# Kernel optimization log

Measured on AMD Instinct MI355X. Metric: run time of the kernel, lower is better.

Reference implementation:

```python
import jax, jax.numpy as jnp
import numpy as np

D_MODEL = 1024
N_HEADS = 16
D_HEAD = D_MODEL // N_HEADS
D_FF = 4096
EPS = 1e-6  # flax LayerNorm default


def setup_inputs() -> dict:
    key = jax.random.key(0)
    ks = jax.random.split(key, 16)
    s = 1.0 / np.sqrt(D_MODEL)
    inp = {
        'x':  jax.random.normal(ks[0], (4, 2048, D_MODEL), jnp.float32),
        'Wq': jax.random.normal(ks[1], (D_MODEL, D_MODEL), jnp.float32) * s,
        'bq': jnp.zeros((D_MODEL,), jnp.float32),
        'Wk': jax.random.normal(ks[2], (D_MODEL, D_MODEL), jnp.float32) * s,
        'bk': jnp.zeros((D_MODEL,), jnp.float32),
        'Wv': jax.random.normal(ks[3], (D_MODEL, D_MODEL), jnp.float32) * s,
        'bv': jnp.zeros((D_MODEL,), jnp.float32),
        'Wo': jax.random.normal(ks[4], (D_MODEL, D_MODEL), jnp.float32) * s,
        'W1': jax.random.normal(ks[5], (D_MODEL, D_FF), jnp.float32) * s,
        'b1': jnp.zeros((D_FF,), jnp.float32),
        'W2': jax.random.normal(ks[6], (D_FF, D_MODEL), jnp.float32) * (1.0 / np.sqrt(D_FF)),
        'b2': jnp.zeros((D_MODEL,), jnp.float32),
        'g1': jnp.ones((D_MODEL,), jnp.float32),
        'beta1': jnp.zeros((D_MODEL,), jnp.float32),
        'g2': jnp.ones((D_MODEL,), jnp.float32),
        'beta2': jnp.zeros((D_MODEL,), jnp.float32),
    }
    return inp


def _layernorm(x, g, b):
    mu = jnp.mean(x, axis=-1, keepdims=True)
    var = jnp.mean(jnp.square(x - mu), axis=-1, keepdims=True)
    return (x - mu) * jax.lax.rsqrt(var + EPS) * g + b


def _attention(x, Wq, bq, Wk, bk, Wv, bv, Wo):
    B, S, D = x.shape
    def split_heads(t):
        return t.reshape(B, S, N_HEADS, D_HEAD).transpose(0, 2, 1, 3)  # bhsd
    q = split_heads(x @ Wq + bq)
    k = split_heads(x @ Wk + bk)
    v = split_heads(x @ Wv + bv)
    scale = jnp.sqrt(jnp.float32(D_HEAD))
    scores = jnp.einsum('bhsd,bhtd->bhst', q, k) / scale
    causal = jnp.tril(jnp.ones((S, S), dtype=jnp.bool_))
    scores = jnp.where(causal, scores, jnp.finfo(scores.dtype).min)
    w = jax.nn.softmax(scores, axis=-1)
    out = jnp.einsum('bhst,bhtd->bhsd', w, v)
    out = out.transpose(0, 2, 1, 3).reshape(B, S, D)
    return out @ Wo  # o_proj has no bias


def reference(x, Wq, bq, Wk, bk, Wv, bv, Wo, W1, b1, W2, b2, g1, beta1, g2, beta2):
    normed = _layernorm(x, g1, beta1)
    x = x + _attention(normed, Wq, bq, Wk, bk, Wv, bv, Wo)
    normed = _layernorm(x, g2, beta2)
    h = jax.nn.gelu(normed @ W1 + b1)  # approximate tanh gelu, matching flax nn.gelu
    x = x + (h @ W2 + b2)
    return x
```

## Files before the change

### kernel.cpp

```cpp
#include <hip/hip_runtime.h>

#define SEQ 2048
#define NROWS 8192
#define NH 16
#define DHEAD 64
#define QLD 3072

typedef float f32x4 __attribute__((ext_vector_type(4)));
typedef __bf16 bf16x8 __attribute__((ext_vector_type(8)));

__device__ __forceinline__ unsigned short f2bf(float f) {
  union { float f; unsigned u; } v; v.f = f;
  unsigned r = v.u + 0x7fffu + ((v.u >> 16) & 1u);
  return (unsigned short)(r >> 16);
}

__device__ __forceinline__ void gl16(const void* g, void* l) {
  __builtin_amdgcn_global_load_lds((const __attribute__((address_space(1))) void*)g,
                                   (__attribute__((address_space(3))) void*)l, 16, 0, 0);
}

__device__ __forceinline__ float gelu_f(float x) {
  float t = 0.7978845608028654f * (x + 0.044715f * x * x * x);
  float e = __expf(2.0f * t);
  float th = 1.0f - 2.0f / (e + 1.0f);
  return 0.5f * x * (1.0f + th);
}

#define CVTPK(dst, lo, hi) asm("v_cvt_pk_bf16_f32 %0, %1, %2" : "=v"(dst) : "v"(lo), "v"(hi))

#if __has_builtin(__builtin_amdgcn_permlane32_swap)
#define P32SWAP(a, b, x, y) { auto _t = __builtin_amdgcn_permlane32_swap((a), (b), false, false); (x) = _t[0]; (y) = _t[1]; }
#else
#define P32SWAP(a, b, x, y) { unsigned _as = (unsigned)__shfl_xor((int)(a), 32, 64); \
  unsigned _bs = (unsigned)__shfl_xor((int)(b), 32, 64); \
  (x) = (l < 32) ? (a) : _bs; (y) = (l < 32) ? _as : (b); }
#endif
#if __has_builtin(__builtin_amdgcn_permlane16_swap)
#define P16SWAP(a, b, x, y) { auto _t = __builtin_amdgcn_permlane16_swap((a), (b), false, false); (x) = _t[0]; (y) = _t[1]; }
#else
#define P16SWAP(a, b, x, y) { unsigned _as = (unsigned)__shfl_xor((int)(a), 16, 64); \
  unsigned _bs = (unsigned)__shfl_xor((int)(b), 16, 64); \
  (x) = (l & 16) ? _bs : (a); (y) = (l & 16) ? (b) : _as; }
#endif

__global__ __launch_bounds__(256) void transpose_cvt(const float* __restrict__ W,
                                                     unsigned short* __restrict__ Wt,
                                                     int K, int N) {
  __shared__ float tile[32][33];
  const int tx = threadIdx.x, ty = threadIdx.y;
  const int n0 = blockIdx.x * 32, k0 = blockIdx.y * 32;
#pragma unroll
  for (int i = ty; i < 32; i += 8)
    tile[i][tx] = W[(size_t)(k0 + i) * N + n0 + tx];
  __syncthreads();
#pragma unroll
  for (int i = ty; i < 32; i += 8)
    Wt[(size_t)(n0 + i) * K + k0 + tx] = f2bf(tile[tx][i]);
}

__global__ __launch_bounds__(256) void concat_bias(const float* __restrict__ bq,
                                                   const float* __restrict__ bk,
                                                   const float* __restrict__ bv,
                                                   float* __restrict__ dst) {
  int i = blockIdx.x * 256 + threadIdx.x;
  if (i < 1024) dst[i] = bq[i];
  else if (i < 2048) dst[i] = bk[i - 1024];
  else if (i < 3072) dst[i] = bv[i - 2048];
}

__global__ __launch_bounds__(256) void layernorm_k(const float* __restrict__ x,
                                                   const float* __restrict__ g,
                                                   const float* __restrict__ b,
                                                   unsigned short* __restrict__ out) {
  const int row = blockIdx.x, tid = threadIdx.x;
  const float4 v = reinterpret_cast<const float4*>(x + (size_t)row * 1024)[tid];
  float s = v.x + v.y + v.z + v.w;
  float s2 = v.x * v.x + v.y * v.y + v.z * v.z + v.w * v.w;
#pragma unroll
  for (int d = 1; d < 64; d <<= 1) { s += __shfl_xor(s, d, 64); s2 += __shfl_xor(s2, d, 64); }
  __shared__ float ls[4], ls2[4];
  const int w = tid >> 6;
  if ((tid & 63) == 0) { ls[w] = s; ls2[w] = s2; }
  __syncthreads();
  s = ls[0] + ls[1] + ls[2] + ls[3];
  s2 = ls2[0] + ls2[1] + ls2[2] + ls2[3];
  const float mu = s * (1.0f / 1024.0f);
  const float var = s2 * (1.0f / 1024.0f) - mu * mu;
  const float rstd = rsqrtf(var + 1e-6f);
  const float4 gv = reinterpret_cast<const float4*>(g)[tid];
  const float4 bv = reinterpret_cast<const float4*>(b)[tid];
  ushort4 o;
  o.x = f2bf((v.x - mu) * rstd * gv.x + bv.x);
  o.y = f2bf((v.y - mu) * rstd * gv.y + bv.y);
  o.z = f2bf((v.z - mu) * rstd * gv.z + bv.z);
  o.w = f2bf((v.w - mu) * rstd * gv.w + bv.w);
  reinterpret_cast<ushort4*>(out + (size_t)row * 1024)[tid] = o;
}

enum { EP_BIAS = 1, EP_RES = 2, EP_GELU = 4, EP_BF16 = 8, EP_QSCALE = 16 };

template <int E>
__global__ __launch_bounds__(256, 2) void gemm_k(const unsigned short* __restrict__ A,
                                                 const unsigned short* __restrict__ Bt,
                                                 const float* __restrict__ bias,
                                                 const float* __restrict__ resid,
                                                 void* __restrict__ out,
                                                 int M, int N, int K) {
  __shared__ __align__(16) unsigned short As[2][128 * 32];
  __shared__ __align__(16) unsigned short Bs[2][128 * 32];
  const int tid = threadIdx.x;
  const int l = tid & 63, w = tid >> 6;
  const int wr = w >> 1, wc = w & 1;
  const int lr = l & 15, lg = l >> 4;
  const int bn = blockIdx.x, bm = blockIdx.y;
  const unsigned short* Ab = A + (size_t)(bm * 128) * K;
  const unsigned short* Bb = Bt + (size_t)(bn * 128) * K;
  const int srow = tid >> 2, scol = (tid & 3) * 8;

  f32x4 acc[4][4];
#pragma unroll
  for (int m = 0; m < 4; ++m)
#pragma unroll
    for (int n = 0; n < 4; ++n) acc[m][n] = 0.0f;

  const int nk = K >> 5;
  auto stage = [&](int buf, int t) {
    const unsigned short* a0 = Ab + (size_t)srow * K + t * 32 + scol;
    const unsigned short* b0 = Bb + (size_t)srow * K + t * 32 + scol;
    gl16(a0, &As[buf][tid * 8]);
    gl16(a0 + (size_t)64 * K, &As[buf][2048 + tid * 8]);
    gl16(b0, &Bs[buf][tid * 8]);
    gl16(b0 + (size_t)64 * K, &Bs[buf][2048 + tid * 8]);
  };
  stage(0, 0);
  for (int t = 0;;) {
    __syncthreads();
    if (t + 1 < nk) stage((t + 1) & 1, t + 1);
    const unsigned short* Ac = As[t & 1];
    const unsigned short* Bc = Bs[t & 1];
    bf16x8 af[4], bfr[4];
#pragma unroll
    for (int m = 0; m < 4; ++m)
      af[m] = *reinterpret_cast<const bf16x8*>(&Ac[(wr * 64 + m * 16 + lr) * 32 + lg * 8]);
#pragma unroll
    for (int n = 0; n < 4; ++n)
      bfr[n] = *reinterpret_cast<const bf16x8*>(&Bc[(wc * 64 + n * 16 + lr) * 32 + lg * 8]);
#pragma unroll
    for (int m = 0; m < 4; ++m)
#pragma unroll
      for (int n = 0; n < 4; ++n)
        acc[m][n] = __builtin_amdgcn_mfma_f32_16x16x32_bf16(af[m], bfr[n], acc[m][n], 0, 0, 0);
    if (++t == nk) break;
  }

  const int row0 = bm * 128 + wr * 64, col0 = bn * 128 + wc * 64;
#pragma unroll
  for (int m = 0; m < 4; ++m) {
#pragma unroll
    for (int n = 0; n < 4; ++n) {
      const int col = col0 + n * 16 + lr;
      float bc = 0.0f;
      if (E & EP_BIAS) bc = bias[col];
#pragma unroll
      for (int j = 0; j < 4; ++j) {
        const int row = row0 + m * 16 + lg * 4 + j;
        float v = acc[m][n][j] + bc;
        if (E & EP_RES) v += resid[(size_t)row * N + col];
        if (E & EP_GELU) v = gelu_f(v);
        if (E & EP_QSCALE) { if (col < 1024) v *= 0.125f; }
        if (E & EP_BF16) ((unsigned short*)out)[(size_t)row * N + col] = f2bf(v);
        else ((float*)out)[(size_t)row * N + col] = v;
      }
    }
  }
}

__global__ __launch_bounds__(512, 4) void attn_k(const unsigned short* __restrict__ qkv,
                                                 unsigned short* __restrict__ out) {
  __shared__ __align__(16) unsigned short Kl[2][4096];
  __shared__ __align__(16) unsigned short Vt[2][4096];
  const int tid = threadIdx.x;
  const int l = tid & 63, w = tid >> 6;
  const int lr = l & 15, lg = l >> 4;
  const int bh = blockIdx.y;
  const int b = bh >> 4, h = bh & 15;
  const size_t rowbase = (size_t)b * SEQ;
  char* klb = (char*)Kl;
  char* vtb = (char*)Vt;
  const int sg = tid & 15, dhg = tid >> 4;

  auto stageK = [&](int buf, int kb2) {
    const int r = (w << 3) + (l >> 3);
    const char* src = (const char*)(qkv + (rowbase + kb2 + r) * QLD + 1024 + h * 64)
                      + 16 * ((l & 7) ^ (l >> 3));
    gl16(src, klb + buf * 8192 + (w << 10) + (l << 4));
  };
  auto loadV = [&](int kb2, uint2* vr) {
    if (tid < 256) {
#pragma unroll
      for (int i = 0; i < 4; ++i)
        vr[i] = *reinterpret_cast<const uint2*>(
            qkv + (rowbase + kb2 + sg * 4 + i) * QLD + 2048 + h * 64 + dhg * 4);
    }
  };
  auto writeV = [&](int buf, const uint2* vr) {
    if (tid < 256) {
      char* vb = vtb + buf * 8192;
#pragma unroll
      for (int jj = 0; jj < 4; ++jj) {
        const int dh = dhg * 4 + jj;
        unsigned a0 = (jj < 2) ? vr[0].x : vr[0].y;
        unsigned a1 = (jj < 2) ? vr[1].x : vr[1].y;
        unsigned a2 = (jj < 2) ? vr[2].x : vr[2].y;
        unsigned a3 = (jj < 2) ? vr[3].x : vr[3].y;
        unsigned s01, s23;
        if (jj & 1) {
          s01 = (a0 >> 16) | (a1 & 0xffff0000u);
          s23 = (a2 >> 16) | (a3 & 0xffff0000u);
        } else {
          s01 = (a0 & 0xffffu) | (a1 << 16);
          s23 = (a2 & 0xffffu) | (a3 << 16);
        }
        const int bo = (dh * 128 + sg * 8) ^ ((dh & 7) << 4);
        uint2 p; p.x = s01; p.y = s23;
        *reinterpret_cast<uint2*>(vb + bo) = p;
      }
    }
  };

#pragma unroll 1
  for (int seg = 0; seg < 2; ++seg) {
    const int qt = seg ? (15 - blockIdx.x) : blockIdx.x;
    const int q0 = qt << 7;
    const int ktmax = 2 * qt + 1;
    const int qwmin = q0 + w * 16;
    const int qrow = qwmin + lr;

    bf16x8 qf[2];
#pragma unroll
    for (int ks = 0; ks < 2; ++ks)
      qf[ks] = *reinterpret_cast<const bf16x8*>(
          qkv + (rowbase + qrow) * QLD + h * 64 + ks * 32 + lg * 8);

    f32x4 oacc[4];
#pragma unroll
    for (int n = 0; n < 4; ++n) oacc[n] = 0.0f;
    float mrun = -1e30f, lrun = 0.0f;

    {
      stageK(0, 0);
      uint2 vr[4];
      loadV(0, vr);
      writeV(0, vr);
    }
    __syncthreads();

#pragma unroll 1
    for (int kt = 0; kt <= ktmax; ++kt) {
      const int cur = kt & 1, nb = cur ^ 1;
      const int kb = kt << 6;
      const bool more = kt < ktmax;
      const bool active = kb <= qwmin + 15;
      uint2 vr[4];
      if (more) { stageK(nb, (kt + 1) << 6); loadV((kt + 1) << 6, vr); }

      f32x4 sacc[4];
      if (active) {
#pragma unroll
        for (int ni = 0; ni < 4; ++ni) sacc[ni] = 0.0f;
        const char* kc = klb + cur * 8192;
        __builtin_amdgcn_s_setprio(1);
#pragma unroll
        for (int ks = 0; ks < 2; ++ks) {
#pragma unroll
          for (int ni = 0; ni < 4; ++ni) {
            const int r = ni * 16 + lr;
            const int bo = (r * 128 + ks * 64 + lg * 16) ^ ((lr & 7) << 4);
            bf16x8 kf = *reinterpret_cast<const bf16x8*>(kc + bo);
            sacc[ni] = __builtin_amdgcn_mfma_f32_16x16x32_bf16(kf, qf[ks], sacc[ni], 0, 0, 0);
          }
        }
        __builtin_amdgcn_s_setprio(0);

        if (kb + 63 > qwmin) {
#pragma unroll
          for (int ni = 0; ni < 4; ++ni)
#pragma unroll
            for (int j = 0; j < 4; ++j)
              if (kb + ni * 16 + lg * 4 + j > qrow) sacc[ni][j] = -1e30f;
        }

        float pm = sacc[0][0];
#pragma unroll
        for (int ni = 0; ni < 4; ++ni)
#pragma unroll
          for (int j = 0; j < 4; ++j) pm = fmaxf(pm, sacc[ni][j]);
        pm = fmaxf(pm, __shfl_xor(pm, 16, 64));
        pm = fmaxf(pm, __shfl_xor(pm, 32, 64));
        const float mnew = fmaxf(mrun, pm);
        const float alpha = __expf(mrun - mnew);
        mrun = mnew;
        float rs = 0.0f;
#pragma unroll
        for (int ni = 0; ni < 4; ++ni)
#pragma unroll
          for (int j = 0; j < 4; ++j) {
            const float p = __expf(sacc[ni][j] - mnew);
            sacc[ni][j] = p;
            rs += p;
          }
        rs += __shfl_xor(rs, 16, 64);
        rs += __shfl_xor(rs, 32, 64);
        lrun = lrun * alpha + rs;
#pragma unroll
        for (int n = 0; n < 4; ++n) oacc[n] *= alpha;
      }

      if (more) writeV(nb, vr);

      if (active) {
        const char* vc = vtb + cur * 8192;
#pragma unroll
        for (int ks2 = 0; ks2 < 2; ++ks2) {
          unsigned U0, U1, U2, U3, C0, C1, W0, W1, W2, W3;
          CVTPK(U0, sacc[2 * ks2][0], sacc[2 * ks2][1]);
          CVTPK(U1, sacc[2 * ks2][2], sacc[2 * ks2][3]);
          CVTPK(U2, sacc[2 * ks2 + 1][0], sacc[2 * ks2 + 1][1]);
          CVTPK(U3, sacc[2 * ks2 + 1][2], sacc[2 * ks2 + 1][3]);
          P32SWAP(U0, U2, C0, C1);
          P16SWAP(C0, C1, W0, W2);
          P32SWAP(U1, U3, C0, C1);
          P16SWAP(C0, C1, W1, W3);
          union { uint4 u; bf16x8 v; } pu;
          pu.u = make_uint4(W0, W1, W2, W3);
          __builtin_amdgcn_s_setprio(1);
#pragma unroll
          for (int n = 0; n < 4; ++n) {
            const int r = n * 16 + lr;
            const int bo = (r * 128 + ks2 * 64 + lg * 16) ^ ((lr & 7) << 4);
            bf16x8 vf = *reinterpret_cast<const bf16x8*>(vc + bo);
            oacc[n] = __builtin_amdgcn_mfma_f32_16x16x32_bf16(vf, pu.v, oacc[n], 0, 0, 0);
          }
          __builtin_amdgcn_s_setprio(0);
        }
      }
      __syncthreads();
    }

    const float inv = 1.0f / lrun;
#pragma unroll
    for (int n = 0; n < 4; ++n) {
      ushort4 o;
      o.x = f2bf(oacc[n][0] * inv);
      o.y = f2bf(oacc[n][1] * inv);
      o.z = f2bf(oacc[n][2] * inv);
      o.w = f2bf(oacc[n][3] * inv);
      *reinterpret_cast<ushort4*>(out + (rowbase + qrow) * 1024 + h * 64 + n * 16 + lg * 4) = o;
    }
  }
}

extern "C" void kernel_launch(void* const* d_in, const int* in_sizes, int n_in,
                              void* d_out, int out_size, void* d_ws, size_t ws_size,
                              hipStream_t stream) {
  const float* x   = (const float*)d_in[0];
  const float* Wq  = (const float*)d_in[1];
  const float* bq  = (const float*)d_in[2];
  const float* Wk  = (const float*)d_in[3];
  const float* bk  = (const float*)d_in[4];
  const float* Wv  = (const float*)d_in[5];
  const float* bv  = (const float*)d_in[6];
  const float* Wo  = (const float*)d_in[7];
  const float* W1  = (const float*)d_in[8];
  const float* b1  = (const float*)d_in[9];
  const float* W2  = (const float*)d_in[10];
  const float* b2  = (const float*)d_in[11];
  const float* g1  = (const float*)d_in[12];
  const float* be1 = (const float*)d_in[13];
  const float* g2  = (const float*)d_in[14];
  const float* be2 = (const float*)d_in[15];

  char* ws = (char*)d_ws;
  size_t off = 0;
  auto alloc = [&](size_t bytes) { char* p = ws + off; off += (bytes + 255) & ~(size_t)255; return p; };
  unsigned short* WqkvT = (unsigned short*)alloc((size_t)3072 * 1024 * 2);
  unsigned short* WoT   = (unsigned short*)alloc((size_t)1024 * 1024 * 2);
  unsigned short* W1T   = (unsigned short*)alloc((size_t)4096 * 1024 * 2);
  unsigned short* W2T   = (unsigned short*)alloc((size_t)1024 * 4096 * 2);
  float*          bqkv  = (float*)alloc((size_t)3072 * 4);
  unsigned short* normed = (unsigned short*)alloc((size_t)NROWS * 1024 * 2);
  unsigned short* qkvbuf = (unsigned short*)alloc((size_t)NROWS * 4096 * 2);
  unsigned short* attnb  = (unsigned short*)alloc((size_t)NROWS * 1024 * 2);
  float*          x1     = (float*)alloc((size_t)NROWS * 1024 * 4);

  const dim3 tb(32, 8);
  transpose_cvt<<<dim3(32, 32), tb, 0, stream>>>(Wq, WqkvT, 1024, 1024);
  transpose_cvt<<<dim3(32, 32), tb, 0, stream>>>(Wk, WqkvT + 1024 * 1024, 1024, 1024);
  transpose_cvt<<<dim3(32, 32), tb, 0, stream>>>(Wv, WqkvT + 2 * 1024 * 1024, 1024, 1024);
  transpose_cvt<<<dim3(32, 32), tb, 0, stream>>>(Wo, WoT, 1024, 1024);
  transpose_cvt<<<dim3(128, 32), tb, 0, stream>>>(W1, W1T, 1024, 4096);
  transpose_cvt<<<dim3(32, 128), tb, 0, stream>>>(W2, W2T, 4096, 1024);
  concat_bias<<<12, 256, 0, stream>>>(bq, bk, bv, bqkv);

  layernorm_k<<<NROWS, 256, 0, stream>>>(x, g1, be1, normed);
  gemm_k<(EP_BIAS | EP_BF16 | EP_QSCALE)><<<dim3(24, 64), 256, 0, stream>>>(normed, WqkvT, bqkv, nullptr, qkvbuf, NROWS, 3072, 1024);
  attn_k<<<dim3(8, 64), 512, 0, stream>>>(qkvbuf, attnb);
  gemm_k<EP_RES><<<dim3(8, 64), 256, 0, stream>>>(attnb, WoT, nullptr, x, x1, NROWS, 1024, 1024);
  layernorm_k<<<NROWS, 256, 0, stream>>>(x1, g2, be2, normed);
  gemm_k<(EP_BIAS | EP_GELU | EP_BF16)><<<dim3(32, 64), 256, 0, stream>>>(normed, W1T, b1, nullptr, qkvbuf, NROWS, 4096, 1024);
  gemm_k<(EP_BIAS | EP_RES)><<<dim3(8, 64), 256, 0, stream>>>(qkvbuf, W2T, b2, x1, d_out, NROWS, 1024, 4096);
}
```

Measured before the change: 553.2 us.

## Replace GEMM with 8-wave 256-row tiled kernel using swizzled LDS and phased pipeline

Replaces the 128x128, 4-wave bf16 GEMM with a 512-thread kernel that uses 256xBN tiles and K-steps of 64. LDS is XOR-swizzled to avoid bank conflicts, and the next tile's global-to-LDS loads are spread across three phases interleaved with MFMA quarters, with raised wave priority during MFMA. Block indices are remapped so that neighbouring workgroups share operands in cache. The aim is more data reuse per byte loaded and better overlap of loads with compute, at the cost of more registers, more LDS and more barriers per iteration.

```diff
diff --git a/kernel.cpp b/kernel.cpp
--- a/kernel.cpp
+++ b/kernel.cpp
@@ -43,6 +43,11 @@
   unsigned _bs = (unsigned)__shfl_xor((int)(b), 16, 64); \
   (x) = (l & 16) ? _bs : (a); (y) = (l & 16) ? (b) : _as; }
 #endif
+
+#define MEMFENCE asm volatile("" ::: "memory")
+#define BAR() do { MEMFENCE; __builtin_amdgcn_s_barrier(); MEMFENCE; } while (0)
+#define WAIT_LGKM0 asm volatile("s_waitcnt lgkmcnt(0)" ::: "memory")
+#define WAIT_VM0 asm volatile("s_waitcnt vmcnt(0)" ::: "memory")
 
 __global__ __launch_bounds__(256) void transpose_cvt(const float* __restrict__ W,
                                                      unsigned short* __restrict__ Wt,
@@ -100,63 +105,158 @@
 
 enum { EP_BIAS = 1, EP_RES = 2, EP_GELU = 4, EP_BF16 = 8, EP_QSCALE = 16 };
 
-template <int E>
-__global__ __launch_bounds__(256, 2) void gemm_k(const unsigned short* __restrict__ A,
-                                                 const unsigned short* __restrict__ Bt,
-                                                 const float* __restrict__ bias,
-                                                 const float* __restrict__ resid,
-                                                 void* __restrict__ out,
-                                                 int M, int N, int K) {
-  __shared__ __align__(16) unsigned short As[2][128 * 32];
-  __shared__ __align__(16) unsigned short Bs[2][128 * 32];
+template <int BN, int E>
+__global__ __launch_bounds__(512, 2) void gemm8_k(const unsigned short* __restrict__ A,
+                                                  const unsigned short* __restrict__ Bt,
+                                                  const float* __restrict__ bias,
+                                                  const float* __restrict__ resid,
+                                                  void* __restrict__ out,
+                                                  int M, int N, int K) {
+  constexpr int BM = 256;
+  constexpr int NWC = (BN == 256) ? 4 : 2;
+  constexpr int WM = (BN == 256) ? 128 : 64;
+  constexpr int MI = WM / 16;
+  constexpr int MQ = MI / 2;
+  __shared__ __align__(16) unsigned short As[2][BM * 64];
+  __shared__ __align__(16) unsigned short Bs[2][BN * 64];
+
   const int tid = threadIdx.x;
   const int l = tid & 63, w = tid >> 6;
-  const int wr = w >> 1, wc = w & 1;
   const int lr = l & 15, lg = l >> 4;
-  const int bn = blockIdx.x, bm = blockIdx.y;
-  const unsigned short* Ab = A + (size_t)(bm * 128) * K;
-  const unsigned short* Bb = Bt + (size_t)(bn * 128) * K;
-  const int srow = tid >> 2, scol = (tid & 3) * 8;
-
-  f32x4 acc[4][4];
-#pragma unroll
-  for (int m = 0; m < 4; ++m)
+  const int wr = w / NWC, wc = w % NWC;
+
+  const int gx = gridDim.x;
+  const int nwg = gx * gridDim.y;
+  int lin = blockIdx.y * gx + blockIdx.x;
+  lin = (lin & 7) * (nwg >> 3) + (lin >> 3);
+  const int bn = lin % gx, bm = lin / gx;
+
+  const unsigned short* Ab = A + (size_t)(bm * BM) * K;
+  const unsigned short* Bb = Bt + (size_t)(bn * BN) * K;
+
+  const int srow = l >> 3;
+  const int sslot = (l & 7) ^ (srow & 7);
+  auto stA = [&](int buf, int t, int seg) {
+    gl16((const char*)(Ab + (size_t)(seg * 8 + srow) * K + t * 64) + sslot * 16,
+         (char*)As[buf] + seg * 1024 + l * 16);
+  };
+  auto stB = [&](int buf, int t, int seg) {
+    gl16((const char*)(Bb + (size_t)(seg * 8 + srow) * K + t * 64) + sslot * 16,
+         (char*)Bs[buf] + seg * 1024 + l * 16);
+  };
+  auto stage = [&](int buf, int t, int p) {
+    if (BN == 256) {
+      if (p == 0)      { stA(buf, t, w); stA(buf, t, 8 + w);  stB(buf, t, w); }
+      else if (p == 1) { stA(buf, t, 16 + w); stA(buf, t, 24 + w); stB(buf, t, 8 + w); }
+      else if (p == 2) { stB(buf, t, 16 + w); stB(buf, t, 24 + w); }
+    } else {
+      if (p == 0)      { stA(buf, t, w); stB(buf, t, w); }
+      else if (p == 1) { stA(buf, t, 8 + w); stB(buf, t, 8 + w); }
+      else if (p == 2) { stA(buf, t, 16 + w); stA(buf, t, 24 + w); }
+    }
+  };
+  auto rdA = [&](int buf, int r, int ks) {
+    return *reinterpret_cast<const bf16x8*>(
+        (const char*)As[buf] + r * 128 + (((ks << 2) + lg) ^ (r & 7)) * 16);
+  };
+  auto rdB = [&](int buf, int r, int ks) {
+    return *reinterpret_cast<const bf16x8*>(
+        (const char*)Bs[buf] + r * 128 + (((ks << 2) + lg) ^ (r & 7)) * 16);
+  };
+
+  f32x4 acc[MI][4];
+#pragma unroll
+  for (int m = 0; m < MI; ++m)
 #pragma unroll
     for (int n = 0; n < 4; ++n) acc[m][n] = 0.0f;
 
-  const int nk = K >> 5;
-  auto stage = [&](int buf, int t) {
-    const unsigned short* a0 = Ab + (size_t)srow * K + t * 32 + scol;
-    const unsigned short* b0 = Bb + (size_t)srow * K + t * 32 + scol;
-    gl16(a0, &As[buf][tid * 8]);
-    gl16(a0 + (size_t)64 * K, &As[buf][2048 + tid * 8]);
-    gl16(b0, &Bs[buf][tid * 8]);
-    gl16(b0 + (size_t)64 * K, &Bs[buf][2048 + tid * 8]);
-  };
-  stage(0, 0);
-  for (int t = 0;;) {
-    __syncthreads();
-    if (t + 1 < nk) stage((t + 1) & 1, t + 1);
-    const unsigned short* Ac = As[t & 1];
-    const unsigned short* Bc = Bs[t & 1];
-    bf16x8 af[4], bfr[4];
-#pragma unroll
-    for (int m = 0; m < 4; ++m)
-      af[m] = *reinterpret_cast<const bf16x8*>(&Ac[(wr * 64 + m * 16 + lr) * 32 + lg * 8]);
-#pragma unroll
-    for (int n = 0; n < 4; ++n)
-      bfr[n] = *reinterpret_cast<const bf16x8*>(&Bc[(wc * 64 + n * 16 + lr) * 32 + lg * 8]);
-#pragma unroll
-    for (int m = 0; m < 4; ++m)
-#pragma unroll
-      for (int n = 0; n < 4; ++n)
-        acc[m][n] = __builtin_amdgcn_mfma_f32_16x16x32_bf16(af[m], bfr[n], acc[m][n], 0, 0, 0);
-    if (++t == nk) break;
+  const int NK = K >> 6;
+#pragma unroll
+  for (int p = 0; p < 3; ++p) stage(0, 0, p);
+  WAIT_VM0;
+  BAR();
+
+#pragma unroll 2
+  for (int kt = 0; kt < NK; ++kt) {
+    const int c = kt & 1, nb = c ^ 1;
+    const bool more = kt + 1 < NK;
+    bf16x8 a0[MQ][2], a1[MQ][2], b0[2][2], b1[2][2];
+
+#pragma unroll
+    for (int mi = 0; mi < MQ; ++mi)
+#pragma unroll
+      for (int ks = 0; ks < 2; ++ks) a0[mi][ks] = rdA(c, wr * WM + mi * 16 + lr, ks);
+#pragma unroll
+    for (int ni = 0; ni < 2; ++ni)
+#pragma unroll
+      for (int ks = 0; ks < 2; ++ks) b0[ni][ks] = rdB(c, wc * 64 + ni * 16 + lr, ks);
+    if (more) stage(nb, kt + 1, 0);
+    BAR();
+    WAIT_LGKM0;
+    __builtin_amdgcn_s_setprio(1);
+#pragma unroll
+    for (int mi = 0; mi < MQ; ++mi)
+#pragma unroll
+      for (int ni = 0; ni < 2; ++ni)
+#pragma unroll
+        for (int ks = 0; ks < 2; ++ks)
+          acc[mi][ni] = __builtin_amdgcn_mfma_f32_16x16x32_bf16(a0[mi][ks], b0[ni][ks], acc[mi][ni], 0, 0, 0);
+    __builtin_amdgcn_s_setprio(0);
+    BAR();
+
+#pragma unroll
+    for (int ni = 0; ni < 2; ++ni)
+#pragma unroll
+      for (int ks = 0; ks < 2; ++ks) b1[ni][ks] = rdB(c, wc * 64 + (2 + ni) * 16 + lr, ks);
+    if (more) stage(nb, kt + 1, 1);
+    BAR();
+    WAIT_LGKM0;
+    __builtin_amdgcn_s_setprio(1);
+#pragma unroll
+    for (int mi = 0; mi < MQ; ++mi)
+#pragma unroll
+      for (int ni = 0; ni < 2; ++ni)
+#pragma unroll
+        for (int ks = 0; ks < 2; ++ks)
+          acc[mi][2 + ni] = __builtin_amdgcn_mfma_f32_16x16x32_bf16(a0[mi][ks], b1[ni][ks], acc[mi][2 + ni], 0, 0, 0);
+    __builtin_amdgcn_s_setprio(0);
+    BAR();
+
+#pragma unroll
+    for (int mi = 0; mi < MQ; ++mi)
+#pragma unroll
+      for (int ks = 0; ks < 2; ++ks) a1[mi][ks] = rdA(c, wr * WM + (MQ + mi) * 16 + lr, ks);
+    if (more) stage(nb, kt + 1, 2);
+    BAR();
+    WAIT_LGKM0;
+    __builtin_amdgcn_s_setprio(1);
+#pragma unroll
+    for (int mi = 0; mi < MQ; ++mi)
+#pragma unroll
+      for (int ni = 0; ni < 2; ++ni)
+#pragma unroll
+        for (int ks = 0; ks < 2; ++ks)
+          acc[MQ + mi][ni] = __builtin_amdgcn_mfma_f32_16x16x32_bf16(a1[mi][ks], b0[ni][ks], acc[MQ + mi][ni], 0, 0, 0);
+    __builtin_amdgcn_s_setprio(0);
+    BAR();
+
+    __builtin_amdgcn_s_setprio(1);
+#pragma unroll
+    for (int mi = 0; mi < MQ; ++mi)
+#pragma unroll
+      for (int ni = 0; ni < 2; ++ni)
+#pragma unroll
+        for (int ks = 0; ks < 2; ++ks)
+          acc[MQ + mi][2 + ni] = __builtin_amdgcn_mfma_f32_16x16x32_bf16(a1[mi][ks], b1[ni][ks], acc[MQ + mi][2 + ni], 0, 0, 0);
+    __builtin_amdgcn_s_setprio(0);
+    WAIT_VM0;
+    BAR();
   }
 
-  const int row0 = bm * 128 + wr * 64, col0 = bn * 128 + wc * 64;
-#pragma unroll
-  for (int m = 0; m < 4; ++m) {
+  const int row0 = bm * BM + wr * WM;
+  const int col0 = bn * BN + wc * 64;
+#pragma unroll
+  for (int m = 0; m < MI; ++m) {
 #pragma unroll
     for (int n = 0; n < 4; ++n) {
       const int col = col0 + n * 16 + lr;
@@ -404,10 +504,10 @@
   concat_bias<<<12, 256, 0, stream>>>(bq, bk, bv, bqkv);
 
   layernorm_k<<<NROWS, 256, 0, stream>>>(x, g1, be1, normed);
-  gemm_k<(EP_BIAS | EP_BF16 | EP_QSCALE)><<<dim3(24, 64), 256, 0, stream>>>(normed, WqkvT, bqkv, nullptr, qkvbuf, NROWS, 3072, 1024);
+  gemm8_k<256, (EP_BIAS | EP_BF16 | EP_QSCALE)><<<dim3(12, 32), 512, 0, stream>>>(normed, WqkvT, bqkv, nullptr, qkvbuf, NROWS, 3072, 1024);
   attn_k<<<dim3(8, 64), 512, 0, stream>>>(qkvbuf, attnb);
-  gemm_k<EP_RES><<<dim3(8, 64), 256, 0, stream>>>(attnb, WoT, nullptr, x, x1, NROWS, 1024, 1024);
+  gemm8_k<128, EP_RES><<<dim3(8, 32), 512, 0, stream>>>(attnb, WoT, nullptr, x, x1, NROWS, 1024, 1024);
   layernorm_k<<<NROWS, 256, 0, stream>>>(x1, g2, be2, normed);
-  gemm_k<(EP_BIAS | EP_GELU | EP_BF16)><<<dim3(32, 64), 256, 0, stream>>>(normed, W1T, b1, nullptr, qkvbuf, NROWS, 4096, 1024);
-  gemm_k<(EP_BIAS | EP_RES)><<<dim3(8, 64), 256, 0, stream>>>(qkvbuf, W2T, b2, x1, d_out, NROWS, 1024, 4096);
-}
+  gemm8_k<256, (EP_BIAS | EP_GELU | EP_BF16)><<<dim3(16, 32), 512, 0, stream>>>(normed, W1T, b1, nullptr, qkvbuf, NROWS, 4096, 1024);
+  gemm8_k<128, (EP_BIAS | EP_RES)><<<dim3(8, 32), 512, 0, stream>>>(qkvbuf, W2T, b2, x1, d_out, NROWS, 1024, 4096);
+}
```

Result: faster. 535.6 us (-3.2%).
